# Performance work log

Measured on AMD Instinct MI355X. Metric: run time of the kernel, lower is better.

Reference implementation:

```python
import jax, jax.numpy as jnp
import numpy as np

D_MODEL = 2048
D_HIDDEN = 8192
EPS = 1e-5


def activation_quant(x):
    # per-token absmax int8 quantization (BitNet b1.58)
    scale = 127.0 / jnp.clip(jnp.max(jnp.abs(x), axis=-1, keepdims=True), EPS, None)
    return jnp.clip(jnp.round(x * scale), -128, 127) / scale


def weight_quant(w):
    # per-tensor ternary quantization with mean-absmax scale
    scale = 1.0 / jnp.clip(jnp.mean(jnp.abs(w)), EPS, None)
    return jnp.clip(jnp.round(w * scale), -1, 1) / scale


def bitlinear(x, w):
    # straight-through estimator around quantizers
    xq = x + jax.lax.stop_gradient(activation_quant(x) - x)
    wq = w + jax.lax.stop_gradient(weight_quant(w) - w)
    # x: [..., in], w: [out, in] (torch F.linear layout)
    return jnp.einsum('bsi,oi->bso', xq, wq)


def setup_inputs() -> dict:
    key = jax.random.key(0)
    k_x, k_w1, k_w2 = jax.random.split(key, 3)
    x = jax.random.normal(k_x, (4, 2048, D_MODEL), dtype=jnp.float32)
    # kaiming-uniform-ish init scale
    w1 = jax.random.normal(k_w1, (D_HIDDEN, D_MODEL), dtype=jnp.float32) * (1.0 / np.sqrt(D_MODEL))
    w2 = jax.random.normal(k_w2, (D_MODEL, D_HIDDEN), dtype=jnp.float32) * (1.0 / np.sqrt(D_HIDDEN))
    return {"x": x, "w1": w1, "w2": w2}


def reference(x, w1, w2):
    h = bitlinear(x, w1)                       # [B, S, d_hidden]
    h = jax.nn.gelu(h, approximate=False)      # nn.GELU() default = exact erf
    return bitlinear(h, w2)                    # [B, S, d_model]
```

## Files before the change

kernel.cpp:

```cpp
#include <hip/hip_runtime.h>
#include <hip/hip_bf16.h>
#include <stdint.h>

#define D_MODEL 2048
#define D_HIDDEN 8192
#define NTOK 8192
#define WELEMS (D_MODEL * D_HIDDEN)

typedef int v4i __attribute__((ext_vector_type(4)));
typedef _Float16 half8 __attribute__((ext_vector_type(8)));

static const size_t OFF_QX  = 0;
static const size_t OFF_QW1 = OFF_QX  + (size_t)NTOK * D_MODEL;
static const size_t OFF_QW2 = OFF_QW1 + (size_t)WELEMS;
static const size_t OFF_QH  = OFF_QW2 + (size_t)WELEMS;
static const size_t OFF_H   = OFF_QH  + (size_t)NTOK * D_HIDDEN;
static const size_t OFF_SXI = OFF_H   + (size_t)NTOK * D_HIDDEN * 2;
static const size_t OFF_SHI = OFF_SXI + (size_t)NTOK * 4;
static const size_t OFF_WP  = OFF_SHI + (size_t)NTOK * 4;
static const size_t OFF_PART= OFF_WP  + 16;

__global__ void wabs_partial(const float* __restrict__ w1, const float* __restrict__ w2,
                             double* __restrict__ part) {
    const int b = blockIdx.x;
    const float* w = (b < 1024) ? w1 : w2;
    const int bb = (b < 1024) ? b : b - 1024;
    const float4* w4 = (const float4*)(w + (size_t)bb * 16384);
    double acc = 0.0;
    for (int i = threadIdx.x; i < 4096; i += 256) {
        float4 v = w4[i];
        acc += (double)fabsf(v.x) + (double)fabsf(v.y) + (double)fabsf(v.z) + (double)fabsf(v.w);
    }
    __shared__ double s[256];
    s[threadIdx.x] = acc;
    __syncthreads();
    for (int st = 128; st > 0; st >>= 1) {
        if (threadIdx.x < st) s[threadIdx.x] += s[threadIdx.x + st];
        __syncthreads();
    }
    if (threadIdx.x == 0) part[b] = s[0];
}

__global__ void wscale_final(const double* __restrict__ part, float* __restrict__ wpar) {
    __shared__ double s[1024];
    const int t = threadIdx.x;
    s[t] = part[t];
    __syncthreads();
    for (int st = 512; st > 0; st >>= 1) { if (t < st) s[t] += s[t + st]; __syncthreads(); }
    double sum1 = s[0];
    __syncthreads();
    s[t] = part[1024 + t];
    __syncthreads();
    for (int st = 512; st > 0; st >>= 1) { if (t < st) s[t] += s[t + st]; __syncthreads(); }
    double sum2 = s[0];
    if (t == 0) {
        float c1 = fmaxf((float)(sum1 / (double)WELEMS), 1e-5f);
        float c2 = fmaxf((float)(sum2 / (double)WELEMS), 1e-5f);
        float s1 = 1.0f / c1, s2 = 1.0f / c2;
        wpar[0] = s1; wpar[1] = 1.0f / s1;
        wpar[2] = s2; wpar[3] = 1.0f / s2;
    }
}

__global__ void quant_w(const float* __restrict__ w1, const float* __restrict__ w2,
                        const float* __restrict__ wpar,
                        int8_t* __restrict__ qw1, int8_t* __restrict__ qw2) {
    const size_t idx = (size_t)blockIdx.x * blockDim.x + threadIdx.x;
    const float* w; int8_t* q; float sc; size_t e;
    if (idx < (size_t)WELEMS / 4) { w = w1; q = qw1; sc = wpar[0]; e = idx * 4; }
    else                          { w = w2; q = qw2; sc = wpar[2]; e = (idx - WELEMS / 4) * 4; }
    float4 v = *(const float4*)(w + e);
    char4 o;
    o.x = (char)fminf(fmaxf(rintf(v.x * sc), -1.f), 1.f);
    o.y = (char)fminf(fmaxf(rintf(v.y * sc), -1.f), 1.f);
    o.z = (char)fminf(fmaxf(rintf(v.z * sc), -1.f), 1.f);
    o.w = (char)fminf(fmaxf(rintf(v.w * sc), -1.f), 1.f);
    *(char4*)(q + e) = o;
}

__global__ void quant_x(const float* __restrict__ x, int8_t* __restrict__ qx,
                        float* __restrict__ sxinv) {
    const int row = blockIdx.x;
    const int t = threadIdx.x;
    const float4* x4 = (const float4*)(x + (size_t)row * D_MODEL);
    float4 a = x4[t * 2], b = x4[t * 2 + 1];
    float vals[8] = {a.x, a.y, a.z, a.w, b.x, b.y, b.z, b.w};
    float m = 0.f;
    #pragma unroll
    for (int i = 0; i < 8; ++i) m = fmaxf(m, fabsf(vals[i]));
    for (int off = 32; off > 0; off >>= 1) m = fmaxf(m, __shfl_xor(m, off, 64));
    __shared__ float s[4];
    if ((t & 63) == 0) s[t >> 6] = m;
    __syncthreads();
    m = fmaxf(fmaxf(s[0], s[1]), fmaxf(s[2], s[3]));
    const float clipv = fmaxf(m, 1e-5f);
    const float scale = 127.0f / clipv;
    if (t == 0) sxinv[row] = 1.0f / scale;
    union { char c[8]; int2 v; } u;
    #pragma unroll
    for (int i = 0; i < 8; ++i) {
        float qv = rintf(vals[i] * scale);
        qv = fminf(fmaxf(qv, -128.f), 127.f);
        u.c[i] = (char)qv;
    }
    *(int2*)(qx + (size_t)row * D_MODEL + t * 8) = u.v;
}

__global__ void quant_h(const _Float16* __restrict__ H, int8_t* __restrict__ qh,
                        float* __restrict__ shinv) {
    const int row = blockIdx.x;
    const int t = threadIdx.x;
    const half8* h8 = (const half8*)(H + (size_t)row * D_HIDDEN) + t * 4;
    half8 v0 = h8[0], v1 = h8[1], v2 = h8[2], v3 = h8[3];
    float vals[32];
    #pragma unroll
    for (int i = 0; i < 8; ++i) {
        vals[i]      = (float)v0[i];
        vals[i + 8]  = (float)v1[i];
        vals[i + 16] = (float)v2[i];
        vals[i + 24] = (float)v3[i];
    }
    float m = 0.f;
    #pragma unroll
    for (int i = 0; i < 32; ++i) m = fmaxf(m, fabsf(vals[i]));
    for (int off = 32; off > 0; off >>= 1) m = fmaxf(m, __shfl_xor(m, off, 64));
    __shared__ float s[4];
    if ((t & 63) == 0) s[t >> 6] = m;
    __syncthreads();
    m = fmaxf(fmaxf(s[0], s[1]), fmaxf(s[2], s[3]));
    const float clipv = fmaxf(m, 1e-5f);
    const float scale = 127.0f / clipv;
    if (t == 0) shinv[row] = 1.0f / scale;
    union { char c[16]; int4 v; } u0, u1;
    #pragma unroll
    for (int i = 0; i < 16; ++i) {
        float qa = rintf(vals[i] * scale);
        qa = fminf(fmaxf(qa, -128.f), 127.f);
        u0.c[i] = (char)qa;
        float qb = rintf(vals[16 + i] * scale);
        qb = fminf(fmaxf(qb, -128.f), 127.f);
        u1.c[i] = (char)qb;
    }
    int4* dst = (int4*)(qh + (size_t)row * D_HIDDEN + t * 32);
    dst[0] = u0.v;
    dst[1] = u1.v;
}

template <int MODE>
__global__ __launch_bounds__(256) void gemm_i8(
    const int8_t* __restrict__ A, const int8_t* __restrict__ B,
    void* __restrict__ Cout, const float* __restrict__ rowinv,
    const float* __restrict__ wdeq, int K, int N) {
    __shared__ __align__(16) int8_t As[128 * 64];
    __shared__ __align__(16) int8_t Bs[128 * 64];
    const int tid = threadIdx.x;
    const int lane = tid & 63;
    const int wid = tid >> 6;
    const int row0 = blockIdx.y * 128;
    const int col0 = blockIdx.x * 128;
    const int wm = (wid >> 1) * 64;
    const int wn = (wid & 1) * 64;
    const int r = lane & 15;
    const int q = lane >> 4;
    v4i acc[4][4] = {};

    for (int k0 = 0; k0 < K; k0 += 64) {
        __syncthreads();
        #pragma unroll
        for (int it = 0; it < 2; ++it) {
            const int o = tid * 16 + it * 4096;
            const int m = o >> 6;
            const int kk = o & 63;
            __builtin_amdgcn_global_load_lds(
                (const __attribute__((address_space(1))) void*)(A + (size_t)(row0 + m) * K + (k0 + kk)),
                (__attribute__((address_space(3))) void*)(As + o), 16, 0, 0);
            __builtin_amdgcn_global_load_lds(
                (const __attribute__((address_space(1))) void*)(B + (size_t)(col0 + m) * K + (k0 + kk)),
                (__attribute__((address_space(3))) void*)(Bs + o), 16, 0, 0);
        }
        __syncthreads();
        v4i af[4], bf[4];
        #pragma unroll
        for (int i = 0; i < 4; ++i)
            af[i] = *(const v4i*)(As + (wm + i * 16 + r) * 64 + q * 16);
        #pragma unroll
        for (int i = 0; i < 4; ++i)
            bf[i] = *(const v4i*)(Bs + (wn + i * 16 + r) * 64 + q * 16);
        #pragma unroll
        for (int mi = 0; mi < 4; ++mi)
            #pragma unroll
            for (int ni = 0; ni < 4; ++ni)
                acc[mi][ni] = __builtin_amdgcn_mfma_i32_16x16x64_i8(af[mi], bf[ni], acc[mi][ni], 0, 0, 0);
    }

    const float dw = *wdeq;
    #pragma unroll
    for (int mi = 0; mi < 4; ++mi) {
        #pragma unroll
        for (int rr = 0; rr < 4; ++rr) {
            const int grow = row0 + wm + mi * 16 + q * 4 + rr;
            const float ri = rowinv[grow] * dw;
            #pragma unroll
            for (int ni = 0; ni < 4; ++ni) {
                const int gcol = col0 + wn + ni * 16 + r;
                float v = (float)acc[mi][ni][rr] * ri;
                if (MODE == 0) {
                    float g = 0.5f * v * (1.0f + erff(v * 0.70710678118654752f));
                    ((_Float16*)Cout)[(size_t)grow * N + gcol] = (_Float16)g;
                } else {
                    ((float*)Cout)[(size_t)grow * N + gcol] = v;
                }
            }
        }
    }
}

extern "C" void kernel_launch(void* const* d_in, const int* in_sizes, int n_in,
                              void* d_out, int out_size, void* d_ws, size_t ws_size,
                              hipStream_t stream) {
    const float* x  = (const float*)d_in[0];
    const float* w1 = (const float*)d_in[1];
    const float* w2 = (const float*)d_in[2];
    float* out = (float*)d_out;
    char* ws = (char*)d_ws;

    int8_t*   qx   = (int8_t*)(ws + OFF_QX);
    int8_t*   qw1  = (int8_t*)(ws + OFF_QW1);
    int8_t*   qw2  = (int8_t*)(ws + OFF_QW2);
    int8_t*   qh   = (int8_t*)(ws + OFF_QH);
    _Float16* h    = (_Float16*)(ws + OFF_H);
    float*    sxi  = (float*)(ws + OFF_SXI);
    float*    shi  = (float*)(ws + OFF_SHI);
    float*    wpar = (float*)(ws + OFF_WP);
    double*   part = (double*)(ws + OFF_PART);

    wabs_partial<<<2048, 256, 0, stream>>>(w1, w2, part);
    wscale_final<<<1, 1024, 0, stream>>>(part, wpar);
    quant_w<<<32768, 256, 0, stream>>>(w1, w2, wpar, qw1, qw2);
    quant_x<<<NTOK, 256, 0, stream>>>(x, qx, sxi);
    gemm_i8<0><<<dim3(D_HIDDEN / 128, NTOK / 128), 256, 0, stream>>>(
        qx, qw1, (void*)h, sxi, wpar + 1, D_MODEL, D_HIDDEN);
    quant_h<<<NTOK, 256, 0, stream>>>(h, qh, shi);
    gemm_i8<1><<<dim3(D_MODEL / 128, NTOK / 128), 256, 0, stream>>>(
        qh, qw2, (void*)out, shi, wpar + 3, D_HIDDEN, D_MODEL);
}
```

Baseline: 719.0 us.

## Double-buffer LDS tiles and XOR-swizzle int8 GEMM shared-memory layout

Converts the int8 MFMA GEMM main loop to a two-stage LDS ping-pong, issuing the global-to-LDS loads for the next K tile before computing on the current one so memory latency overlaps with MFMA work. It also applies an XOR swizzle to the 16-byte chunk placement in LDS, matched on the read side, to reduce bank conflicts when loading fragments. LDS usage doubles to 32 KB per block, which may lower occupancy, and the loop assumes K is a multiple of 128.

```diff
diff --git a/kernel.cpp b/kernel.cpp
--- a/kernel.cpp
+++ b/kernel.cpp
@@ -151,8 +151,8 @@
     const int8_t* __restrict__ A, const int8_t* __restrict__ B,
     void* __restrict__ Cout, const float* __restrict__ rowinv,
     const float* __restrict__ wdeq, int K, int N) {
-    __shared__ __align__(16) int8_t As[128 * 64];
-    __shared__ __align__(16) int8_t Bs[128 * 64];
+    __shared__ __align__(16) int8_t As[2][128 * 64];
+    __shared__ __align__(16) int8_t Bs[2][128 * 64];
     const int tid = threadIdx.x;
     const int lane = tid & 63;
     const int wid = tid >> 6;
@@ -162,36 +162,67 @@
     const int wn = (wid & 1) * 64;
     const int r = lane & 15;
     const int q = lane >> 4;
+
+    const int sm = tid >> 2;
+    const int sc = tid & 3;
+    const int swk = ((sc ^ ((sm >> 2) & 3)) << 4);
+    const int8_t* gA0 = A + (size_t)(row0 + sm) * K + swk;
+    const int8_t* gA1 = gA0 + (size_t)64 * K;
+    const int8_t* gB0 = B + (size_t)(col0 + sm) * K + swk;
+    const int8_t* gB1 = gB0 + (size_t)64 * K;
+    const int ldso = tid * 16;
+
+#define STAGE(pA, pB, kk)                                                              \
+    do {                                                                               \
+        __builtin_amdgcn_global_load_lds(                                              \
+            (const __attribute__((address_space(1))) void*)(gA0 + (kk)),               \
+            (__attribute__((address_space(3))) void*)((pA) + ldso), 16, 0, 0);         \
+        __builtin_amdgcn_global_load_lds(                                              \
+            (const __attribute__((address_space(1))) void*)(gA1 + (kk)),               \
+            (__attribute__((address_space(3))) void*)((pA) + ldso + 4096), 16, 0, 0);  \
+        __builtin_amdgcn_global_load_lds(                                              \
+            (const __attribute__((address_space(1))) void*)(gB0 + (kk)),               \
+            (__attribute__((address_space(3))) void*)((pB) + ldso), 16, 0, 0);         \
+        __builtin_amdgcn_global_load_lds(                                              \
+            (const __attribute__((address_space(1))) void*)(gB1 + (kk)),               \
+            (__attribute__((address_space(3))) void*)((pB) + ldso + 4096), 16, 0, 0);  \
+    } while (0)
+
+    int aoff[4], boff[4];
+    const int rchunk = (q ^ (r >> 2)) << 4;
+    #pragma unroll
+    for (int i = 0; i < 4; ++i) {
+        aoff[i] = (wm + i * 16 + r) * 64 + rchunk;
+        boff[i] = (wn + i * 16 + r) * 64 + rchunk;
+    }
+
     v4i acc[4][4] = {};
 
-    for (int k0 = 0; k0 < K; k0 += 64) {
+#define COMPUTE(pA, pB)                                                                 \
+    do {                                                                                \
+        v4i af[4], bf[4];                                                               \
+        _Pragma("unroll") for (int i = 0; i < 4; ++i) {                                 \
+            af[i] = *(const v4i*)((pA) + aoff[i]);                                      \
+            bf[i] = *(const v4i*)((pB) + boff[i]);                                      \
+        }                                                                               \
+        _Pragma("unroll") for (int mi = 0; mi < 4; ++mi)                                \
+            _Pragma("unroll") for (int ni = 0; ni < 4; ++ni)                            \
+                acc[mi][ni] =                                                           \
+                    __builtin_amdgcn_mfma_i32_16x16x64_i8(af[mi], bf[ni], acc[mi][ni],  \
+                                                          0, 0, 0);                     \
+    } while (0)
+
+    STAGE(As[0], Bs[0], 0);
+    for (int k0 = 0; k0 < K; k0 += 128) {
         __syncthreads();
-        #pragma unroll
-        for (int it = 0; it < 2; ++it) {
-            const int o = tid * 16 + it * 4096;
-            const int m = o >> 6;
-            const int kk = o & 63;
-            __builtin_amdgcn_global_load_lds(
-                (const __attribute__((address_space(1))) void*)(A + (size_t)(row0 + m) * K + (k0 + kk)),
-                (__attribute__((address_space(3))) void*)(As + o), 16, 0, 0);
-            __builtin_amdgcn_global_load_lds(
-                (const __attribute__((address_space(1))) void*)(B + (size_t)(col0 + m) * K + (k0 + kk)),
-                (__attribute__((address_space(3))) void*)(Bs + o), 16, 0, 0);
-        }
+        if (k0 + 64 < K) STAGE(As[1], Bs[1], k0 + 64);
+        COMPUTE(As[0], Bs[0]);
         __syncthreads();
-        v4i af[4], bf[4];
-        #pragma unroll
-        for (int i = 0; i < 4; ++i)
-            af[i] = *(const v4i*)(As + (wm + i * 16 + r) * 64 + q * 16);
-        #pragma unroll
-        for (int i = 0; i < 4; ++i)
-            bf[i] = *(const v4i*)(Bs + (wn + i * 16 + r) * 64 + q * 16);
-        #pragma unroll
-        for (int mi = 0; mi < 4; ++mi)
-            #pragma unroll
-            for (int ni = 0; ni < 4; ++ni)
-                acc[mi][ni] = __builtin_amdgcn_mfma_i32_16x16x64_i8(af[mi], bf[ni], acc[mi][ni], 0, 0, 0);
-    }
+        if (k0 + 128 < K) STAGE(As[0], Bs[0], k0 + 128);
+        COMPUTE(As[1], Bs[1]);
+    }
+#undef STAGE
+#undef COMPUTE
 
     const float dw = *wdeq;
     #pragma unroll
```

Result: faster. 669.1 us (-6.9%).
